# Optimization experiments

Hardware: AMD Instinct MI355X
Metric: run time of the kernel (lower is better)

## Reference

```python
import jax, jax.numpy as jnp
import numpy as np

B, NCAMS = 1, 6
C_FEAT = 64                     # fusion_feat_in_dim
H, W = 88, 160                  # per-camera feature map size at fusion level
VOX_SIZE = (100, 100, 20)       # (x_dim, y_dim, z_dim) voxel counts
VOX_STR = (-50.0, -50.0, -15.0)
VOX_UNIT = (1.0, 1.0, 1.5)
N_VOX = VOX_SIZE[0] * VOX_SIZE[1] * VOX_SIZE[2]
EPS = 1e-8
V_PRE = 64                      # voxel_pre_dim[0]


def make_voxel_pts(dtype):
    # [B, 4, N]; homogeneous (x, y, z, 1) points, layout [z, y, x] flattened
    xs = jnp.linspace(VOX_STR[0], VOX_STR[0] + VOX_UNIT[0] * (VOX_SIZE[0] - 1), VOX_SIZE[0], dtype=dtype)
    ys = jnp.linspace(VOX_STR[1], VOX_STR[1] + VOX_UNIT[1] * (VOX_SIZE[1] - 1), VOX_SIZE[1], dtype=dtype)
    zs = jnp.linspace(VOX_STR[2], VOX_STR[2] + VOX_UNIT[2] * (VOX_SIZE[2] - 1), VOX_SIZE[2], dtype=dtype)
    zdim, ydim, xdim = VOX_SIZE[2], VOX_SIZE[1], VOX_SIZE[0]
    gx = jnp.broadcast_to(xs[None, None, :], (zdim, ydim, xdim)).reshape(-1)
    gy = jnp.broadcast_to(ys[None, :, None], (zdim, ydim, xdim)).reshape(-1)
    gz = jnp.broadcast_to(zs[:, None, None], (zdim, ydim, xdim)).reshape(-1)
    pts = jnp.stack([gx, gy, gz, jnp.ones_like(gx)], axis=0)  # [4, N]
    return jnp.broadcast_to(pts[None], (B, 4, N_VOX))


def _gather(imgf, iy, ix, Wd):
    # imgf: [BN, C, H*W]; iy/ix: [BN, N] int32 -> [BN, C, N]
    lin = iy * Wd + ix
    return jnp.take_along_axis(imgf, lin[:, None, :], axis=2)


def bilinear_sample(img, gx, gy):
    # grid_sample(mode='bilinear', padding_mode='zeros', align_corners=True)
    BN, C, Hd, Wd = img.shape
    x = (gx + 1.0) * 0.5 * (Wd - 1)
    y = (gy + 1.0) * 0.5 * (Hd - 1)
    x0 = jnp.floor(x); y0 = jnp.floor(y)
    wx1 = x - x0; wx0 = 1.0 - wx1
    wy1 = y - y0; wy0 = 1.0 - wy1
    imgf = img.reshape(BN, C, Hd * Wd)
    out = jnp.zeros((BN, C, gx.shape[1]), dtype=img.dtype)
    for xi, wxi in ((x0, wx0), (x0 + 1.0, wx1)):
        for yi, wyi in ((y0, wy0), (y0 + 1.0, wy1)):
            valid = (xi >= 0) & (xi <= Wd - 1) & (yi >= 0) & (yi <= Hd - 1)
            ii = jnp.clip(xi, 0, Wd - 1).astype(jnp.int32)
            jj = jnp.clip(yi, 0, Hd - 1).astype(jnp.int32)
            w = (wxi * wyi * valid.astype(img.dtype))[:, None, :]
            out = out + _gather(imgf, jj, ii, Wd) * w
    return out


def nearest_sample(img, gx, gy):
    # grid_sample(mode='nearest', padding_mode='zeros', align_corners=True)
    BN, C, Hd, Wd = img.shape
    x = (gx + 1.0) * 0.5 * (Wd - 1)
    y = (gy + 1.0) * 0.5 * (Hd - 1)
    xi = jnp.round(x); yi = jnp.round(y)
    valid = (xi >= 0) & (xi <= Wd - 1) & (yi >= 0) & (yi <= Hd - 1)
    ii = jnp.clip(xi, 0, Wd - 1).astype(jnp.int32)
    jj = jnp.clip(yi, 0, Hd - 1).astype(jnp.int32)
    imgf = img.reshape(BN, C, Hd * Wd)
    return _gather(imgf, jj, ii, Wd) * valid[:, None, :].astype(img.dtype)


def setup_inputs() -> dict:
    key = jax.random.key(0)
    ks = jax.random.split(key, 8)
    return {
        'multi_img_feat': jax.random.normal(ks[0], (B, NCAMS, C_FEAT, H, W), jnp.float32),
        'mask': jax.random.uniform(ks[1], (B, NCAMS, 1, H, W), jnp.float32),
        'K': jax.random.normal(ks[2], (B, NCAMS, 4, 4), jnp.float32),
        'extrinsics': jax.random.normal(ks[3], (B, NCAMS, 4, 4), jnp.float32),
        'w_no': jax.random.normal(ks[4], (V_PRE, C_FEAT + 1), jnp.float32) * 0.05,
        'b_no': jax.random.normal(ks[5], (V_PRE,), jnp.float32) * 0.05,
        'w_o': jax.random.normal(ks[6], (V_PRE, 2 * (C_FEAT + 1)), jnp.float32) * 0.05,
        'b_o': jax.random.normal(ks[7], (V_PRE,), jnp.float32) * 0.05,
    }


def reference(multi_img_feat, mask, K, extrinsics, w_no, b_no, w_o, b_o):
    Bb, NC, C, Hd, Wd = multi_img_feat.shape
    dt = multi_img_feat.dtype
    vpts = make_voxel_pts(dt)                                          # [B,4,N]
    vpts_c = jnp.broadcast_to(vpts[:, None], (Bb, NC, 4, N_VOX)).reshape(Bb * NC, 4, N_VOX)
    feats = multi_img_feat.reshape(Bb * NC, C, Hd, Wd)
    masks = mask.reshape(Bb * NC, 1, Hd, Wd)                           # interp to (H,W) is identity (same size, align_corners)
    ext = extrinsics.reshape(Bb * NC, 4, 4)[:, :3, :]
    K3 = K.reshape(Bb * NC, 4, 4)[:, :3, :3]

    v_local = jnp.einsum('bij,bjn->bin', ext, vpts_c)                  # [BN,3,N]
    cam_pts = jnp.einsum('bij,bjn->bin', K3, v_local)
    pix = cam_pts[:, :2] / (cam_pts[:, 2:3] + EPS)
    pix = jnp.where(jnp.all(jnp.isfinite(pix)), pix, jnp.clip(pix, -Wd * 2.0, Wd * 2.0))
    gx = (pix[:, 0] / (Wd - 1) - 0.5) * 2.0                            # [BN,N] normalized coords
    gy = (pix[:, 1] / (Hd - 1) - 0.5) * 2.0

    feat_w = bilinear_sample(feats, gx, gy)                            # [BN,C,N]
    m_occ = nearest_sample(masks, gx, gy) > 0.5                        # [BN,1,N]
    m_depth = v_local[:, 2:3] > 0
    oob = (gx > 1) | (gx < -1) | (gy > 1) | (gy < -1)
    valid = (m_occ & m_depth & (~oob)[:, None, :]).astype(dt)          # [BN,1,N]

    feat_w = jnp.concatenate([feat_w, v_local[:, 2:3] / VOX_SIZE[0]], axis=1) * valid  # [BN,C+1,N]

    feat_w = feat_w.reshape(Bb, NC, C + 1, N_VOX)
    valid = valid.reshape(Bb, NC, 1, N_VOX)
    count = valid.sum(axis=1)                                          # [B,1,N]

    # non-overlap branch: voxels seen by exactly one camera
    no_mask = (count == 1).astype(dt)
    vox_no = feat_w.sum(axis=1) * no_mask
    vox_no = jax.nn.elu(jnp.einsum('oc,bcn->bon', w_no, vox_no) + b_no[None, :, None]) * no_mask

    # overlap branch: cams {0,3,4} vs {1,2,5}
    o_mask = (count == 2).astype(dt)
    feat1 = feat_w[:, 0] + feat_w[:, 3] + feat_w[:, 4]
    feat2 = feat_w[:, 1] + feat_w[:, 2] + feat_w[:, 5]
    vox_o = jnp.concatenate([feat1, feat2], axis=1)                    # [B,2*(C+1),N]
    vox_o = jax.nn.elu(jnp.einsum('oc,bcn->bon', w_o, vox_o) + b_o[None, :, None]) * o_mask

    return vox_no + vox_o                                              # [B, V_PRE, N]
```

## Files before the change

### kernel.cpp

```cpp
#include <hip/hip_runtime.h>
#include <cmath>

#define NC 6
#define CF 64
#define HH 88
#define WW 160
#define NPIX 14080
#define NVOX 200000
#define VPRE 64
#define VB 128
#define NTH 512
#define NWV 8

typedef unsigned int u32;

#define FEATT_BYTES  (6u * 64u * 14080u * 4u)

__global__ __launch_bounds__(256) void transpose_feats(const float* __restrict__ in,
                                                       float* __restrict__ out) {
    __shared__ float tile[64 * 65];
    int blk = blockIdx.x;
    int c = blk / 220;
    int p0 = (blk - c * 220) * 64;
    int tid = threadIdx.x;
    int lane = tid & 63;
    int quad = tid >> 6;
    for (int r = quad; r < 64; r += 4)
        tile[r * 65 + lane] = in[(c * 64 + r) * NPIX + p0 + lane];
    __syncthreads();
    for (int r = quad; r < 64; r += 4)
        out[((c * NPIX) + p0 + r) * 64 + lane] = tile[lane * 65 + r];
}

__device__ __forceinline__ float elu1(float x) { return x > 0.0f ? x : expm1f(x); }

__device__ __forceinline__ float gather_bilin(const float* __restrict__ fsrc, int useT,
                                              int lane, int cam, float x, float y) {
    float x0f = floorf(x), y0f = floorf(y);
    float wx1 = x - x0f, wx0 = 1.0f - wx1;
    float wy1 = y - y0f, wy0 = 1.0f - wy1;
    float x1f = x0f + 1.0f, y1f = y0f + 1.0f;
    float bx0 = (x0f >= 0.0f && x0f <= 159.0f) ? 1.0f : 0.0f;
    float bx1 = (x1f >= 0.0f && x1f <= 159.0f) ? 1.0f : 0.0f;
    float by0 = (y0f >= 0.0f && y0f <= 87.0f) ? 1.0f : 0.0f;
    float by1 = (y1f >= 0.0f && y1f <= 87.0f) ? 1.0f : 0.0f;
    int ix0 = (int)fminf(fmaxf(x0f, 0.0f), 159.0f);
    int ix1 = (int)fminf(fmaxf(x1f, 0.0f), 159.0f);
    int iy0 = (int)fminf(fmaxf(y0f, 0.0f), 87.0f);
    int iy1 = (int)fminf(fmaxf(y1f, 0.0f), 87.0f);
    int A = useT ? 64 : 1;
    int Boff = useT ? (cam * NPIX * 64 + lane) : ((cam * 64 + lane) * NPIX);
    float v00 = fsrc[(iy0 * WW + ix0) * A + Boff];
    float v01 = fsrc[(iy1 * WW + ix0) * A + Boff];
    float v10 = fsrc[(iy0 * WW + ix1) * A + Boff];
    float v11 = fsrc[(iy1 * WW + ix1) * A + Boff];
    float fv;
    fv  = (wx0 * wy0 * bx0 * by0) * v00;
    fv += (wx0 * wy1 * bx0 * by1) * v01;
    fv += (wx1 * wy0 * bx1 * by0) * v10;
    fv += (wx1 * wy1 * bx1 * by1) * v11;
    return fv;
}

#define FMA8_STEP(W0,W1,W2,W3,W4,W5,W6,W7,CG,F0,F1,F2,F3) \
    a0 += W0[CG]*F0; a0 += W0[CG+1]*F1; a0 += W0[CG+2]*F2; a0 += W0[CG+3]*F3; \
    a1 += W1[CG]*F0; a1 += W1[CG+1]*F1; a1 += W1[CG+2]*F2; a1 += W1[CG+3]*F3; \
    a2 += W2[CG]*F0; a2 += W2[CG+1]*F1; a2 += W2[CG+2]*F2; a2 += W2[CG+3]*F3; \
    a3 += W3[CG]*F0; a3 += W3[CG+1]*F1; a3 += W3[CG+2]*F2; a3 += W3[CG+3]*F3; \
    a4 += W4[CG]*F0; a4 += W4[CG+1]*F1; a4 += W4[CG+2]*F2; a4 += W4[CG+3]*F3; \
    a5 += W5[CG]*F0; a5 += W5[CG+1]*F1; a5 += W5[CG+2]*F2; a5 += W5[CG+3]*F3; \
    a6 += W6[CG]*F0; a6 += W6[CG+1]*F1; a6 += W6[CG+2]*F2; a6 += W6[CG+3]*F3; \
    a7 += W7[CG]*F0; a7 += W7[CG+1]*F1; a7 += W7[CG+2]*F2; a7 += W7[CG+3]*F3;

#define STORE8(COL) \
    outp[(size_t)(obase + 0) * NVOX + COL] = elu1(a0); \
    outp[(size_t)(obase + 1) * NVOX + COL] = elu1(a1); \
    outp[(size_t)(obase + 2) * NVOX + COL] = elu1(a2); \
    outp[(size_t)(obase + 3) * NVOX + COL] = elu1(a3); \
    outp[(size_t)(obase + 4) * NVOX + COL] = elu1(a4); \
    outp[(size_t)(obase + 5) * NVOX + COL] = elu1(a5); \
    outp[(size_t)(obase + 6) * NVOX + COL] = elu1(a6); \
    outp[(size_t)(obase + 7) * NVOX + COL] = elu1(a7);

__global__ __launch_bounds__(NTH) void vox_fused(
    const float* __restrict__ feats,
    const float* __restrict__ featT,
    const float* __restrict__ mask,
    const float* __restrict__ Kg,
    const float* __restrict__ ext,
    const float* __restrict__ wno,
    const float* __restrict__ bno,
    const float* __restrict__ wo,
    const float* __restrict__ bo,
    float* __restrict__ outp,
    int useT)
{
    __shared__ float s_ext[72];
    __shared__ float s_K[54];
    __shared__ float s_F[65 * 66];
    __shared__ __align__(16) float4 s_rec1[VB];
    __shared__ __align__(16) float4 s_rec2[2 * VB];
    __shared__ int s_vox[64];
    __shared__ int s_n1, s_n2;

    int tid = threadIdx.x;
    int lane = tid & 63;
    int wv = tid >> 6;
    int base = blockIdx.x * VB;
    int vlim = min(VB, NVOX - base);

    if (tid == 0) { s_n1 = 0; s_n2 = 0; }
    if (tid >= 64 && tid < 136) {
        int i = tid - 64;
        s_ext[i] = ext[(i / 12) * 16 + (i % 12)];
    }
    if (tid >= 192 && tid < 246) {
        int i = tid - 192; int cam = i / 9; int e = i - cam * 9;
        s_K[i] = Kg[cam * 16 + (e / 3) * 4 + (e % 3)];
    }

    {
        int ng4 = vlim >> 2;
        for (int i = tid; i < 64 * (VB / 4); i += NTH) {
            int r = i >> 5, cg = i & ((VB / 4) - 1);
            if (cg < ng4)
                *(float4*)(outp + (size_t)r * NVOX + base + (cg << 2)) =
                    make_float4(0.f, 0.f, 0.f, 0.f);
        }
    }
    __syncthreads();

    if (tid < vlim) {
        #pragma clang fp contract(off)
        int n = base + tid;
        int xi = n % 100;
        int t = n / 100;
        int yi = t % 100;
        int zi = t / 100;
        float X = -50.0f + (float)xi;
        float Y = -50.0f + (float)yi;
        float Z = -15.0f + 1.5f * (float)zi;
        int cnt = 0, cam0 = 0, cam1 = 0;
        float ax = 0.f, ay = 0.f, az = 0.f, bx = 0.f, by = 0.f, bz = 0.f;
        #pragma unroll
        for (int cam = 0; cam < NC; ++cam) {
            const float* E = s_ext + cam * 12;
            const float* Kk = s_K + cam * 9;
            float vl0 = E[0]*X + E[1]*Y + E[2]*Z + E[3];
            float vl1 = E[4]*X + E[5]*Y + E[6]*Z + E[7];
            float vl2 = E[8]*X + E[9]*Y + E[10]*Z + E[11];
            float c0 = Kk[0]*vl0 + Kk[1]*vl1 + Kk[2]*vl2;
            float c1 = Kk[3]*vl0 + Kk[4]*vl1 + Kk[5]*vl2;
            float c2 = Kk[6]*vl0 + Kk[7]*vl1 + Kk[8]*vl2;
            float pz = c2 + 1e-8f;
            float px = c0 / pz;
            float py = c1 / pz;
            float gx = (px / 159.0f - 0.5f) * 2.0f;
            float gy = (py / 87.0f - 0.5f) * 2.0f;
            float x = ((gx + 1.0f) * 0.5f) * 159.0f;
            float y = ((gy + 1.0f) * 0.5f) * 87.0f;
            float xr = rintf(x), yr = rintf(y);
            bool nv = (xr >= 0.0f) && (xr <= 159.0f) && (yr >= 0.0f) && (yr <= 87.0f);
            float mval = 0.0f;
            if (nv) mval = mask[(cam * HH + (int)yr) * WW + (int)xr];
            bool ok = (mval > 0.5f) && (vl2 > 0.0f) &&
                      !((gx > 1.0f) || (gx < -1.0f) || (gy > 1.0f) || (gy < -1.0f));
            if (ok) {
                if (cnt == 0) { ax = x; ay = y; az = vl2; cam0 = cam; }
                else if (cnt == 1) { bx = x; by = y; bz = vl2; cam1 = cam; }
                ++cnt;
            }
        }
        if (cnt == 1) {
            int s = atomicAdd(&s_n1, 1);
            s_rec1[s] = make_float4(ax, ay, az, __int_as_float((n << 3) | cam0));
        } else if (cnt == 2) {
            int s = atomicAdd(&s_n2, 1);
            s_rec2[2 * s + 0] = make_float4(ax, ay, az, __int_as_float((n << 3) | cam0));
            s_rec2[2 * s + 1] = make_float4(bx, by, bz, __int_as_float((n << 3) | cam1));
        }
    }
    __syncthreads();

    int n1 = s_n1, n2 = s_n2;
    const float* fsrc = useT ? featT : feats;
    int wvu = __builtin_amdgcn_readfirstlane(wv);
    int obase = wvu * 8;
    const float* w0n = wno + (obase + 0) * 65;
    const float* w1n = wno + (obase + 1) * 65;
    const float* w2n = wno + (obase + 2) * 65;
    const float* w3n = wno + (obase + 3) * 65;
    const float* w4n = wno + (obase + 4) * 65;
    const float* w5n = wno + (obase + 5) * 65;
    const float* w6n = wno + (obase + 6) * 65;
    const float* w7n = wno + (obase + 7) * 65;
    const float* w0o = wo + (obase + 0) * 130;
    const float* w1o = wo + (obase + 1) * 130;
    const float* w2o = wo + (obase + 2) * 130;
    const float* w3o = wo + (obase + 3) * 130;
    const float* w4o = wo + (obase + 4) * 130;
    const float* w5o = wo + (obase + 5) * 130;
    const float* w6o = wo + (obase + 6) * 130;
    const float* w7o = wo + (obase + 7) * 130;

    for (int t0 = 0; t0 < n1; t0 += 64) {
        int tl = min(64, n1 - t0);
        for (int e = wv; e < tl; e += NWV) {
            float4 r = s_rec1[t0 + e];
            int meta = __float_as_int(r.w);
            int cam = meta & 7;
            float fv = gather_bilin(fsrc, useT, lane, cam, r.x, r.y);
            s_F[lane * 66 + e] = fv;
            if (lane == 0) { s_F[64 * 66 + e] = r.z / 100.0f; s_vox[e] = meta >> 3; }
        }
        __syncthreads();
        float a0 = bno[obase + 0], a1 = bno[obase + 1], a2 = bno[obase + 2], a3 = bno[obase + 3];
        float a4 = bno[obase + 4], a5 = bno[obase + 5], a6 = bno[obase + 6], a7 = bno[obase + 7];
        for (int cg = 0; cg < 64; cg += 4) {
            float f0 = s_F[(cg + 0) * 66 + lane];
            float f1 = s_F[(cg + 1) * 66 + lane];
            float f2 = s_F[(cg + 2) * 66 + lane];
            float f3 = s_F[(cg + 3) * 66 + lane];
            FMA8_STEP(w0n, w1n, w2n, w3n, w4n, w5n, w6n, w7n, cg, f0, f1, f2, f3)
        }
        float fd = s_F[64 * 66 + lane];
        a0 += w0n[64] * fd; a1 += w1n[64] * fd; a2 += w2n[64] * fd; a3 += w3n[64] * fd;
        a4 += w4n[64] * fd; a5 += w5n[64] * fd; a6 += w6n[64] * fd; a7 += w7n[64] * fd;
        if (lane < tl) {
            size_t col = (size_t)s_vox[lane];
            STORE8(col)
        }
        __syncthreads();
    }

    for (int t0 = 0; t0 < n2; t0 += 64) {
        int tl = min(64, n2 - t0);
        for (int e = wv; e < tl; e += NWV) {
            float4 r0 = s_rec2[2 * (t0 + e) + 0];
            float4 r1 = s_rec2[2 * (t0 + e) + 1];
            int m0 = __float_as_int(r0.w), m1 = __float_as_int(r1.w);
            int ca = m0 & 7, cb = m1 & 7;
            float fg = 0.0f, dd = 0.0f;
            if (!(ca == 1 || ca == 2 || ca == 5)) {
                fg += gather_bilin(fsrc, useT, lane, ca, r0.x, r0.y);
                dd += r0.z / 100.0f;
            }
            if (!(cb == 1 || cb == 2 || cb == 5)) {
                fg += gather_bilin(fsrc, useT, lane, cb, r1.x, r1.y);
                dd += r1.z / 100.0f;
            }
            s_F[lane * 66 + e] = fg;
            if (lane == 0) { s_F[64 * 66 + e] = dd; s_vox[e] = m0 >> 3; }
        }
        __syncthreads();
        float a0 = bo[obase + 0], a1 = bo[obase + 1], a2 = bo[obase + 2], a3 = bo[obase + 3];
        float a4 = bo[obase + 4], a5 = bo[obase + 5], a6 = bo[obase + 6], a7 = bo[obase + 7];
        for (int cg = 0; cg < 64; cg += 4) {
            float f0 = s_F[(cg + 0) * 66 + lane];
            float f1 = s_F[(cg + 1) * 66 + lane];
            float f2 = s_F[(cg + 2) * 66 + lane];
            float f3 = s_F[(cg + 3) * 66 + lane];
            FMA8_STEP(w0o, w1o, w2o, w3o, w4o, w5o, w6o, w7o, cg, f0, f1, f2, f3)
        }
        {
            float fd = s_F[64 * 66 + lane];
            a0 += w0o[64] * fd; a1 += w1o[64] * fd; a2 += w2o[64] * fd; a3 += w3o[64] * fd;
            a4 += w4o[64] * fd; a5 += w5o[64] * fd; a6 += w6o[64] * fd; a7 += w7o[64] * fd;
        }
        __syncthreads();
        for (int e = wv; e < tl; e += NWV) {
            float4 r0 = s_rec2[2 * (t0 + e) + 0];
            float4 r1 = s_rec2[2 * (t0 + e) + 1];
            int m0 = __float_as_int(r0.w), m1 = __float_as_int(r1.w);
            int ca = m0 & 7, cb = m1 & 7;
            float fg = 0.0f, dd = 0.0f;
            if (ca == 1 || ca == 2 || ca == 5) {
                fg += gather_bilin(fsrc, useT, lane, ca, r0.x, r0.y);
                dd += r0.z / 100.0f;
            }
            if (cb == 1 || cb == 2 || cb == 5) {
                fg += gather_bilin(fsrc, useT, lane, cb, r1.x, r1.y);
                dd += r1.z / 100.0f;
            }
            s_F[lane * 66 + e] = fg;
            if (lane == 0) s_F[64 * 66 + e] = dd;
        }
        __syncthreads();
        for (int cg = 0; cg < 64; cg += 4) {
            float f0 = s_F[(cg + 0) * 66 + lane];
            float f1 = s_F[(cg + 1) * 66 + lane];
            float f2 = s_F[(cg + 2) * 66 + lane];
            float f3 = s_F[(cg + 3) * 66 + lane];
            int cgo = cg + 65;
            FMA8_STEP(w0o, w1o, w2o, w3o, w4o, w5o, w6o, w7o, cgo, f0, f1, f2, f3)
        }
        {
            float fd = s_F[64 * 66 + lane];
            a0 += w0o[129] * fd; a1 += w1o[129] * fd; a2 += w2o[129] * fd; a3 += w3o[129] * fd;
            a4 += w4o[129] * fd; a5 += w5o[129] * fd; a6 += w6o[129] * fd; a7 += w7o[129] * fd;
        }
        if (lane < tl) {
            size_t col = (size_t)s_vox[lane];
            STORE8(col)
        }
        __syncthreads();
    }
}

extern "C" void kernel_launch(void* const* d_in, const int* in_sizes, int n_in,
                              void* d_out, int out_size, void* d_ws, size_t ws_size,
                              hipStream_t stream) {
    const float* feats = (const float*)d_in[0];
    const float* mask  = (const float*)d_in[1];
    const float* Kg    = (const float*)d_in[2];
    const float* ext   = (const float*)d_in[3];
    const float* wno   = (const float*)d_in[4];
    const float* bno   = (const float*)d_in[5];
    const float* wo    = (const float*)d_in[6];
    const float* bo    = (const float*)d_in[7];
    float* outp = (float*)d_out;
    float* featT = (float*)d_ws;

    int useT = (ws_size >= (size_t)FEATT_BYTES) ? 1 : 0;
    if (useT) {
        transpose_feats<<<NC * 220, 256, 0, stream>>>(feats, featT);
    }
    int nblk = (NVOX + VB - 1) / VB;
    vox_fused<<<nblk, NTH, 0, stream>>>(feats, featT, mask, Kg, ext,
                                        wno, bno, wo, bo, outp, useT);
}
```

Before: 161.9 us.

## Split voxel pipeline into geometry compaction and compacted compute kernels

Adds a geometry kernel that projects each voxel into all cameras, zero-fills the outputs of voxels seen by zero or more than two cameras, and compacts the one-camera and two-camera voxels into record lists using block-local then global atomics. A second persistent kernel then gathers bilinear features and runs the 65- or 130-wide matvec only for the compacted voxels, in tiles of 64. The aim is to stop spending gather and matmul work on the many voxels whose output is zero. The cost is an extra launch, workspace traffic for the records, scattered output writes, and a larger workspace requirement, with the old fused path kept as a fallback.

```diff
diff --git a/kernel.cpp b/kernel.cpp
--- a/kernel.cpp
+++ b/kernel.cpp
@@ -15,10 +15,16 @@
 typedef unsigned int u32;
 
 #define FEATT_BYTES  (6u * 64u * 14080u * 4u)
+#define CNT_OFF      (((FEATT_BYTES) + 255u) & ~255u)
+#define REC1_OFF     (CNT_OFF + 256u)
+#define REC2_OFF     (REC1_OFF + (u32)NVOX * 16u)
+#define WS_NEED      ((size_t)REC2_OFF + (size_t)NVOX * 32u)
 
 __global__ __launch_bounds__(256) void transpose_feats(const float* __restrict__ in,
-                                                       float* __restrict__ out) {
+                                                       float* __restrict__ out,
+                                                       int* __restrict__ cnt) {
     __shared__ float tile[64 * 65];
+    if (cnt && blockIdx.x == 0 && threadIdx.x < 2) cnt[threadIdx.x] = 0;
     int blk = blockIdx.x;
     int c = blk / 220;
     int p0 = (blk - c * 220) * 64;
@@ -60,6 +66,257 @@
     fv += (wx1 * wy0 * bx1 * by0) * v10;
     fv += (wx1 * wy1 * bx1 * by1) * v11;
     return fv;
+}
+
+__global__ __launch_bounds__(256) void vox_geom(
+    const float* __restrict__ mask,
+    const float* __restrict__ Kg,
+    const float* __restrict__ ext,
+    float* __restrict__ outp,
+    float4* __restrict__ rec1,
+    float4* __restrict__ rec2,
+    int* __restrict__ cnt)
+{
+    __shared__ float s_ext[72];
+    __shared__ float s_K[54];
+    __shared__ float4 s_r1[256];
+    __shared__ float4 s_r2[512];
+    __shared__ int s_c1, s_c2, s_b1, s_b2;
+
+    int tid = threadIdx.x;
+    if (tid == 0) { s_c1 = 0; s_c2 = 0; }
+    if (tid >= 64 && tid < 136) {
+        int i = tid - 64;
+        s_ext[i] = ext[(i / 12) * 16 + (i % 12)];
+    }
+    if (tid >= 160 && tid < 214) {
+        int i = tid - 160; int cam = i / 9; int e = i - cam * 9;
+        s_K[i] = Kg[cam * 16 + (e / 3) * 4 + (e % 3)];
+    }
+    __syncthreads();
+
+    int n = blockIdx.x * 256 + tid;
+    if (n < NVOX) {
+        #pragma clang fp contract(off)
+        int xi = n % 100;
+        int t = n / 100;
+        int yi = t % 100;
+        int zi = t / 100;
+        float X = -50.0f + (float)xi;
+        float Y = -50.0f + (float)yi;
+        float Z = -15.0f + 1.5f * (float)zi;
+        int cc = 0, cam0 = 0, cam1 = 0;
+        float ax = 0.f, ay = 0.f, az = 0.f, bx = 0.f, by = 0.f, bz = 0.f;
+        #pragma unroll
+        for (int cam = 0; cam < NC; ++cam) {
+            const float* E = s_ext + cam * 12;
+            const float* Kk = s_K + cam * 9;
+            float vl0 = E[0]*X + E[1]*Y + E[2]*Z + E[3];
+            float vl1 = E[4]*X + E[5]*Y + E[6]*Z + E[7];
+            float vl2 = E[8]*X + E[9]*Y + E[10]*Z + E[11];
+            float c0 = Kk[0]*vl0 + Kk[1]*vl1 + Kk[2]*vl2;
+            float c1 = Kk[3]*vl0 + Kk[4]*vl1 + Kk[5]*vl2;
+            float c2 = Kk[6]*vl0 + Kk[7]*vl1 + Kk[8]*vl2;
+            float pz = c2 + 1e-8f;
+            float px = c0 / pz;
+            float py = c1 / pz;
+            float gx = (px / 159.0f - 0.5f) * 2.0f;
+            float gy = (py / 87.0f - 0.5f) * 2.0f;
+            float x = ((gx + 1.0f) * 0.5f) * 159.0f;
+            float y = ((gy + 1.0f) * 0.5f) * 87.0f;
+            float xr = rintf(x), yr = rintf(y);
+            bool nv = (xr >= 0.0f) && (xr <= 159.0f) && (yr >= 0.0f) && (yr <= 87.0f);
+            float mval = 0.0f;
+            if (nv) mval = mask[(cam * HH + (int)yr) * WW + (int)xr];
+            bool ok = (mval > 0.5f) && (vl2 > 0.0f) &&
+                      !((gx > 1.0f) || (gx < -1.0f) || (gy > 1.0f) || (gy < -1.0f));
+            if (ok) {
+                if (cc == 0) { ax = x; ay = y; az = vl2; cam0 = cam; }
+                else if (cc == 1) { bx = x; by = y; bz = vl2; cam1 = cam; }
+                ++cc;
+            }
+        }
+        if (cc == 1) {
+            int s = atomicAdd(&s_c1, 1);
+            s_r1[s] = make_float4(ax, ay, az, __int_as_float((n << 3) | cam0));
+        } else if (cc == 2) {
+            int s = atomicAdd(&s_c2, 1);
+            s_r2[2 * s + 0] = make_float4(ax, ay, az, __int_as_float((n << 3) | cam0));
+            s_r2[2 * s + 1] = make_float4(bx, by, bz, __int_as_float((n << 3) | cam1));
+        } else {
+            #pragma unroll 8
+            for (int r = 0; r < 64; ++r)
+                outp[(size_t)r * NVOX + n] = 0.0f;
+        }
+    }
+    __syncthreads();
+    if (tid == 0) {
+        s_b1 = atomicAdd(cnt + 0, s_c1);
+        s_b2 = atomicAdd(cnt + 1, s_c2);
+    }
+    __syncthreads();
+    int c1 = s_c1, c2 = s_c2, b1 = s_b1, b2 = s_b2;
+    for (int i = tid; i < c1; i += 256) rec1[b1 + i] = s_r1[i];
+    for (int i = tid; i < 2 * c2; i += 256) rec2[2 * b2 + i] = s_r2[i];
+}
+
+__global__ __launch_bounds__(256) void vox_comp(
+    const float* __restrict__ featT,
+    const float* __restrict__ wno,
+    const float* __restrict__ bno,
+    const float* __restrict__ wo,
+    const float* __restrict__ bo,
+    float* __restrict__ outp,
+    const float4* __restrict__ rec1,
+    const float4* __restrict__ rec2,
+    const int* __restrict__ cnt)
+{
+    __shared__ float s_F[65 * 66];
+    __shared__ float4 s_rec[128];
+    __shared__ int s_vox[64];
+
+    int tid = threadIdx.x;
+    int lane = tid & 63;
+    int wv = tid >> 6;
+    int wvu = __builtin_amdgcn_readfirstlane(wv);
+    int obase = wvu * 16;
+
+    int n1 = cnt[0], n2 = cnt[1];
+    int T1 = (n1 + 63) >> 6;
+    int T2 = (n2 + 63) >> 6;
+    int TT = T1 + T2;
+
+    for (int t = blockIdx.x; t < TT; t += gridDim.x) {
+        if (t < T1) {
+            int e0 = t << 6;
+            int tl = min(64, n1 - e0);
+            if (tid < tl) s_rec[tid] = rec1[e0 + tid];
+            __syncthreads();
+            for (int e = wv; e < tl; e += 4) {
+                float4 r = s_rec[e];
+                int meta = __float_as_int(r.w);
+                int cam = meta & 7;
+                float fv = gather_bilin(featT, 1, lane, cam, r.x, r.y);
+                s_F[lane * 66 + e] = fv;
+                if (lane == 0) { s_F[64 * 66 + e] = r.z / 100.0f; s_vox[e] = meta >> 3; }
+            }
+            __syncthreads();
+            float acc[16];
+            #pragma unroll
+            for (int o = 0; o < 16; ++o) acc[o] = bno[obase + o];
+            for (int cg = 0; cg < 64; cg += 4) {
+                float f0 = s_F[(cg + 0) * 66 + lane];
+                float f1 = s_F[(cg + 1) * 66 + lane];
+                float f2 = s_F[(cg + 2) * 66 + lane];
+                float f3 = s_F[(cg + 3) * 66 + lane];
+                #pragma unroll
+                for (int o = 0; o < 16; ++o) {
+                    const float* wr = wno + (obase + o) * 65 + cg;
+                    acc[o] += wr[0] * f0; acc[o] += wr[1] * f1;
+                    acc[o] += wr[2] * f2; acc[o] += wr[3] * f3;
+                }
+            }
+            {
+                float fd = s_F[64 * 66 + lane];
+                #pragma unroll
+                for (int o = 0; o < 16; ++o) acc[o] += wno[(obase + o) * 65 + 64] * fd;
+            }
+            if (lane < tl) {
+                size_t col = (size_t)s_vox[lane];
+                #pragma unroll
+                for (int o = 0; o < 16; ++o)
+                    outp[(size_t)(obase + o) * NVOX + col] = elu1(acc[o]);
+            }
+            __syncthreads();
+        } else {
+            int tt = t - T1;
+            int e0 = tt << 6;
+            int tl = min(64, n2 - e0);
+            if (tid < 2 * tl) s_rec[tid] = rec2[2 * e0 + tid];
+            __syncthreads();
+            for (int e = wv; e < tl; e += 4) {
+                float4 r0 = s_rec[2 * e + 0];
+                float4 r1 = s_rec[2 * e + 1];
+                int m0 = __float_as_int(r0.w), m1 = __float_as_int(r1.w);
+                int ca = m0 & 7, cb = m1 & 7;
+                float fg = 0.0f, dd = 0.0f;
+                if (!(ca == 1 || ca == 2 || ca == 5)) {
+                    fg += gather_bilin(featT, 1, lane, ca, r0.x, r0.y);
+                    dd += r0.z / 100.0f;
+                }
+                if (!(cb == 1 || cb == 2 || cb == 5)) {
+                    fg += gather_bilin(featT, 1, lane, cb, r1.x, r1.y);
+                    dd += r1.z / 100.0f;
+                }
+                s_F[lane * 66 + e] = fg;
+                if (lane == 0) { s_F[64 * 66 + e] = dd; s_vox[e] = m0 >> 3; }
+            }
+            __syncthreads();
+            float acc[16];
+            #pragma unroll
+            for (int o = 0; o < 16; ++o) acc[o] = bo[obase + o];
+            for (int cg = 0; cg < 64; cg += 4) {
+                float f0 = s_F[(cg + 0) * 66 + lane];
+                float f1 = s_F[(cg + 1) * 66 + lane];
+                float f2 = s_F[(cg + 2) * 66 + lane];
+                float f3 = s_F[(cg + 3) * 66 + lane];
+                #pragma unroll
+                for (int o = 0; o < 16; ++o) {
+                    const float* wr = wo + (obase + o) * 130 + cg;
+                    acc[o] += wr[0] * f0; acc[o] += wr[1] * f1;
+                    acc[o] += wr[2] * f2; acc[o] += wr[3] * f3;
+                }
+            }
+            {
+                float fd = s_F[64 * 66 + lane];
+                #pragma unroll
+                for (int o = 0; o < 16; ++o) acc[o] += wo[(obase + o) * 130 + 64] * fd;
+            }
+            __syncthreads();
+            for (int e = wv; e < tl; e += 4) {
+                float4 r0 = s_rec[2 * e + 0];
+                float4 r1 = s_rec[2 * e + 1];
+                int m0 = __float_as_int(r0.w), m1 = __float_as_int(r1.w);
+                int ca = m0 & 7, cb = m1 & 7;
+                float fg = 0.0f, dd = 0.0f;
+                if (ca == 1 || ca == 2 || ca == 5) {
+                    fg += gather_bilin(featT, 1, lane, ca, r0.x, r0.y);
+                    dd += r0.z / 100.0f;
+                }
+                if (cb == 1 || cb == 2 || cb == 5) {
+                    fg += gather_bilin(featT, 1, lane, cb, r1.x, r1.y);
+                    dd += r1.z / 100.0f;
+                }
+                s_F[lane * 66 + e] = fg;
+                if (lane == 0) s_F[64 * 66 + e] = dd;
+            }
+            __syncthreads();
+            for (int cg = 0; cg < 64; cg += 4) {
+                float f0 = s_F[(cg + 0) * 66 + lane];
+                float f1 = s_F[(cg + 1) * 66 + lane];
+                float f2 = s_F[(cg + 2) * 66 + lane];
+                float f3 = s_F[(cg + 3) * 66 + lane];
+                #pragma unroll
+                for (int o = 0; o < 16; ++o) {
+                    const float* wr = wo + (obase + o) * 130 + 65 + cg;
+                    acc[o] += wr[0] * f0; acc[o] += wr[1] * f1;
+                    acc[o] += wr[2] * f2; acc[o] += wr[3] * f3;
+                }
+            }
+            {
+                float fd = s_F[64 * 66 + lane];
+                #pragma unroll
+                for (int o = 0; o < 16; ++o) acc[o] += wo[(obase + o) * 130 + 129] * fd;
+            }
+            if (lane < tl) {
+                size_t col = (size_t)s_vox[lane];
+                #pragma unroll
+                for (int o = 0; o < 16; ++o)
+                    outp[(size_t)(obase + o) * NVOX + col] = elu1(acc[o]);
+            }
+            __syncthreads();
+        }
+    }
 }
 
 #define FMA8_STEP(W0,W1,W2,W3,W4,W5,W6,W7,CG,F0,F1,F2,F3) \
@@ -321,11 +578,22 @@
     float* outp = (float*)d_out;
     float* featT = (float*)d_ws;
 
-    int useT = (ws_size >= (size_t)FEATT_BYTES) ? 1 : 0;
-    if (useT) {
-        transpose_feats<<<NC * 220, 256, 0, stream>>>(feats, featT);
-    }
-    int nblk = (NVOX + VB - 1) / VB;
-    vox_fused<<<nblk, NTH, 0, stream>>>(feats, featT, mask, Kg, ext,
-                                        wno, bno, wo, bo, outp, useT);
+    if (ws_size >= WS_NEED) {
+        int* cnt = (int*)((char*)d_ws + CNT_OFF);
+        float4* rec1 = (float4*)((char*)d_ws + REC1_OFF);
+        float4* rec2 = (float4*)((char*)d_ws + REC2_OFF);
+        transpose_feats<<<NC * 220, 256, 0, stream>>>(feats, featT, cnt);
+        vox_geom<<<(NVOX + 255) / 256, 256, 0, stream>>>(mask, Kg, ext, outp,
+                                                         rec1, rec2, cnt);
+        vox_comp<<<2048, 256, 0, stream>>>(featT, wno, bno, wo, bo, outp,
+                                           rec1, rec2, cnt);
+    } else {
+        int useT = (ws_size >= (size_t)FEATT_BYTES) ? 1 : 0;
+        if (useT) {
+            transpose_feats<<<NC * 220, 256, 0, stream>>>(feats, featT, nullptr);
+        }
+        int nblk = (NVOX + VB - 1) / VB;
+        vox_fused<<<nblk, NTH, 0, stream>>>(feats, featT, mask, Kg, ext,
+                                            wno, bno, wo, bo, outp, useT);
+    }
 }
```

Result: slower. 176.1 us (+8.8%).
